# Performance work log

Measured on AMD Instinct MI355X. Metric: run time of the kernel, lower is better.

## Reference

```python
import jax, jax.numpy as jnp
import numpy as np
from jax import lax

K_NN = 16      # neighbors used by compute_knn_distance
ANCHOR_K = 64  # config['anchor_k']


def _knn_dist_vec(pts):
    """compute_knn_distance for one object: mean offset vector to K_NN nearest neighbors.
    pts: (N, 3) -> (N, 3)"""
    sq = jnp.sum(pts * pts, axis=-1)                      # (N,)
    d2 = sq[:, None] + sq[None, :] - 2.0 * (pts @ pts.T)  # (N, N) squared dists
    n = pts.shape[0]
    d2 = d2 + jnp.eye(n, dtype=pts.dtype) * 1e10          # exclude self
    _, idx = lax.top_k(-d2, K_NN)                          # (N, K_NN) nearest indices
    neigh = pts[idx]                                       # (N, K_NN, 3)
    return jnp.mean(neigh - pts[:, None, :], axis=1)       # (N, 3)


def _fps(pts, k):
    """Farthest point sampling for one object. pts: (N, 3) -> (k,) int32 indices."""
    d0 = jnp.sum((pts - pts[0]) ** 2, axis=-1)             # dist to seed point 0

    def step(min_d, _):
        idx = jnp.argmax(min_d)
        d = jnp.sum((pts - pts[idx]) ** 2, axis=-1)
        return jnp.minimum(min_d, d), idx

    _, idxs = lax.scan(step, d0, None, length=k - 1)
    return jnp.concatenate([jnp.zeros((1,), dtype=idxs.dtype), idxs])


def setup_inputs() -> dict:
    key = jax.random.key(0)
    k1, k2, k3, k4 = jax.random.split(key, 4)
    B, N_obj, N_v = 4, 8, 2048
    positions = jax.random.normal(k1, (B, N_obj, N_v, 3), dtype=jnp.float32)
    velocities = jax.random.normal(k2, (B, N_obj, N_v, 3), dtype=jnp.float32)
    physics_params = jax.random.uniform(k3, (B, N_obj, 3), dtype=jnp.float32)
    # reference pose at t=0: nearby but distinct so rel_pos is nontrivial
    ref_positions = positions + 0.05 * jax.random.normal(k4, (B, N_obj, N_v, 3), dtype=jnp.float32)
    return {"positions": positions, "velocities": velocities,
            "physics_params": physics_params, "ref_positions": ref_positions}


def reference(positions, velocities, physics_params, ref_positions):
    B, N_obj, N_v, _ = positions.shape
    flat = positions.reshape(B * N_obj, N_v, 3)

    # pairwise KNN distance feature per point
    dist_vec = jax.vmap(_knn_dist_vec)(flat).reshape(B, N_obj, N_v, 3)

    # iterative FPS anchor sampling (vectorized over all B*N_obj objects)
    anchors = jax.vmap(lambda p: _fps(p, ANCHOR_K))(flat).reshape(B, N_obj, ANCHOR_K)

    rel_pos = positions - ref_positions

    # multi-field gather at anchor indices (torch.gather on dim=2)
    gather = lambda f: jnp.take_along_axis(f, anchors[..., None], axis=2)
    anchor_dist = gather(dist_vec)       # (B, N_obj, K, 3)
    anchor_vel = gather(velocities)      # (B, N_obj, K, 3)
    anchor_rel = gather(rel_pos)         # (B, N_obj, K, 3)

    phys = jnp.broadcast_to(physics_params[:, :, None, :], (B, N_obj, ANCHOR_K, 3))
    query = jnp.concatenate([anchor_dist, anchor_vel, anchor_rel, phys], axis=-1)  # (B, N_obj, K, 12)
    return query
```

## Files before the change

kernel.cpp:

```cpp
#include <hip/hip_runtime.h>
#include <stdint.h>

#define NPTS 2048
#define KNN  16
#define AK   64
#define TPB  256
#define FPT  (NPTS / TPB)
#define KPL  (NPTS / 64)

typedef unsigned long long u64;
typedef unsigned int u32;
#define UMAX 0xFFFFFFFFFFFFFFFFull

__device__ __forceinline__ float sq3(float x, float y, float z) {
    return __fadd_rn(__fadd_rn(__fmul_rn(x, x), __fmul_rn(y, y)), __fmul_rn(z, z));
}

template <int CTRL>
__device__ __forceinline__ u64 dpp64(u64 k) {
    const int lo = __builtin_amdgcn_update_dpp((int)(u32)k, (int)(u32)k,
                                               CTRL, 0xF, 0xF, false);
    const int hi = __builtin_amdgcn_update_dpp((int)(u32)(k >> 32),
                                               (int)(u32)(k >> 32),
                                               CTRL, 0xF, 0xF, false);
    return ((u64)(u32)hi << 32) | (u32)lo;
}

__device__ __forceinline__ u64 wave_max64(u64 k) {
    u64 o;
    o = dpp64<0xB1>(k);  if (o > k) k = o;
    o = dpp64<0x4E>(k);  if (o > k) k = o;
    o = dpp64<0x141>(k); if (o > k) k = o;
    o = dpp64<0x140>(k); if (o > k) k = o;
    o = (u64)__shfl_xor((long long)k, 16, 64); if (o > k) k = o;
    o = (u64)__shfl_xor((long long)k, 32, 64); if (o > k) k = o;
    return k;
}

__device__ __forceinline__ u64 wave_min64(u64 k) {
    u64 o;
    o = dpp64<0xB1>(k);  if (o < k) k = o;
    o = dpp64<0x4E>(k);  if (o < k) k = o;
    o = dpp64<0x141>(k); if (o < k) k = o;
    o = dpp64<0x140>(k); if (o < k) k = o;
    o = (u64)__shfl_xor((long long)k, 16, 64); if (o < k) k = o;
    o = (u64)__shfl_xor((long long)k, 32, 64); if (o < k) k = o;
    return k;
}

__global__ __launch_bounds__(TPB) void fps_kernel(const float* __restrict__ pos,
                                                  int* __restrict__ anchors) {
    const int obj = blockIdx.x;
    const int t = threadIdx.x;
    const int wid = t >> 6, lane = t & 63;

    __shared__ float sX[NPTS], sY[NPTS], sZ[NPTS];
    __shared__ u64 skey[8];
    __shared__ float4 scrd[8];

    const float* pts = pos + (size_t)obj * NPTS * 3;
    #pragma unroll
    for (int i = 0; i < FPT; i++) {
        const int j = t + i * TPB;
        sX[j] = pts[j * 3 + 0];
        sY[j] = pts[j * 3 + 1];
        sZ[j] = pts[j * 3 + 2];
    }
    __syncthreads();

    float px[FPT], py[FPT], pz[FPT], mind[FPT];
    u64 key;
    {
        const float ax0 = sX[0], ay0 = sY[0], az0 = sZ[0];
        float bv = -1.0f; u32 bj = 0;
        #pragma unroll
        for (int i = 0; i < FPT; i++) {
            const int j = t + i * TPB;
            px[i] = sX[j]; py[i] = sY[j]; pz[i] = sZ[j];
            const float d2 = sq3(__fsub_rn(px[i], ax0), __fsub_rn(py[i], ay0),
                                 __fsub_rn(pz[i], az0));
            mind[i] = d2;
            if (d2 > bv) { bv = d2; bj = (u32)j; }
        }
        key = ((u64)__float_as_uint(bv) << 32) | (u32)(~bj);
    }
    if (t == 0) anchors[obj * AK + 0] = 0;

    for (int s = 1; s < AK; s++) {
        const u64 wk = wave_max64(key);
        const int side = (s & 1) * 4;
        if (lane == 0) {
            const int widx = (int)(~(u32)wk);
            skey[side + wid] = wk;
            scrd[side + wid] = make_float4(sX[widx], sY[widx], sZ[widx], 0.f);
        }
        __syncthreads();
        u64 ka = skey[side + 0];
        float4 ca = scrd[side + 0];
        { const u64 k1 = skey[side + 1]; const float4 q = scrd[side + 1];
          if (k1 > ka) { ka = k1; ca = q; } }
        { const u64 k2 = skey[side + 2]; const float4 q = scrd[side + 2];
          if (k2 > ka) { ka = k2; ca = q; } }
        { const u64 k3 = skey[side + 3]; const float4 q = scrd[side + 3];
          if (k3 > ka) { ka = k3; ca = q; } }
        if (t == 0) anchors[obj * AK + s] = (int)(~(u32)ka);
        if (s == AK - 1) break;

        float bv = -1.0f; u32 bj = 0;
        #pragma unroll
        for (int i = 0; i < FPT; i++) {
            const float d2 = sq3(__fsub_rn(px[i], ca.x), __fsub_rn(py[i], ca.y),
                                 __fsub_rn(pz[i], ca.z));
            const float nm = fminf(mind[i], d2);
            mind[i] = nm;
            if (nm > bv) { bv = nm; bj = (u32)(t + i * TPB); }
        }
        key = ((u64)__float_as_uint(bv) << 32) | (u32)(~bj);
    }
}

__global__ __launch_bounds__(TPB) void knn_gather_kernel(
    const float* __restrict__ pos, const float* __restrict__ vel,
    const float* __restrict__ phys, const float* __restrict__ refp,
    const int* __restrict__ anchors, float* __restrict__ out) {
    const int t = threadIdx.x;
    const int wid = t >> 6, lane = t & 63;
    const int g = blockIdx.x * 4 + wid;
    const int obj = g >> 6;

    __shared__ float sX[NPTS], sY[NPTS], sZ[NPTS];
    const float* pts = pos + (size_t)obj * NPTS * 3;
    #pragma unroll
    for (int i = 0; i < FPT; i++) {
        const int j = t + i * TPB;
        sX[j] = pts[j * 3 + 0];
        sY[j] = pts[j * 3 + 1];
        sZ[j] = pts[j * 3 + 2];
    }
    const int a = anchors[g];
    __syncthreads();

    const float ax = sX[a], ay = sY[a], az = sZ[a];
    const float sqa = sq3(ax, ay, az);

    u64 k[KPL];
    #pragma unroll
    for (int i = 0; i < KPL; i++) {
        const int j = lane + i * 64;
        const float x = sX[j], y = sY[j], z = sZ[j];
        const float sqj = sq3(x, y, z);
        const float dot = __fadd_rn(
            __fadd_rn(__fmul_rn(ax, x), __fmul_rn(ay, y)), __fmul_rn(az, z));
        const float d2 = __fsub_rn(__fadd_rn(sqa, sqj), __fmul_rn(2.0f, dot));
        u32 bb = __float_as_uint(d2);
        bb ^= (bb & 0x80000000u) ? 0xFFFFFFFFu : 0x80000000u;
        k[i] = (j == a) ? UMAX : (((u64)bb << 32) | (u32)j);
    }

    u64 c0 = UMAX, c1 = UMAX, c2 = UMAX, c3 = UMAX;
    #pragma unroll
    for (int i = 0; i < KPL; i++) c0 = (k[i] < c0) ? k[i] : c0;
    #pragma unroll
    for (int i = 0; i < KPL; i++) {
        const u64 v = (k[i] > c0) ? k[i] : UMAX; c1 = (v < c1) ? v : c1;
    }
    #pragma unroll
    for (int i = 0; i < KPL; i++) {
        const u64 v = (k[i] > c1) ? k[i] : UMAX; c2 = (v < c2) ? v : c2;
    }
    #pragma unroll
    for (int i = 0; i < KPL; i++) {
        const u64 v = (k[i] > c2) ? k[i] : UMAX; c3 = (v < c3) ? v : c3;
    }

    float accx = 0.f, accy = 0.f, accz = 0.f;
    u64 thr = 0;
    for (int r = 0; r < KNN; r++) {
        if (c0 == UMAX) {
            #pragma unroll
            for (int i = 0; i < KPL; i++) {
                const u64 v = (k[i] > thr) ? k[i] : UMAX; c0 = (v < c0) ? v : c0;
            }
            #pragma unroll
            for (int i = 0; i < KPL; i++) {
                const u64 v = (k[i] > c0) ? k[i] : UMAX; c1 = (v < c1) ? v : c1;
            }
            #pragma unroll
            for (int i = 0; i < KPL; i++) {
                const u64 v = (k[i] > c1) ? k[i] : UMAX; c2 = (v < c2) ? v : c2;
            }
            #pragma unroll
            for (int i = 0; i < KPL; i++) {
                const u64 v = (k[i] > c2) ? k[i] : UMAX; c3 = (v < c3) ? v : c3;
            }
        }
        const u64 w = wave_min64(c0);
        const int winj = (int)(u32)w;
        const float wx = sX[winj], wy = sY[winj], wz = sZ[winj];
        accx = __fadd_rn(accx, __fsub_rn(wx, ax));
        accy = __fadd_rn(accy, __fsub_rn(wy, ay));
        accz = __fadd_rn(accz, __fsub_rn(wz, az));
        if (c0 == w) {
            thr = c0; c0 = c1; c1 = c2; c2 = c3; c3 = UMAX;
        }
    }

    if (lane == 0) {
        float* o = out + (size_t)g * 12;
        o[0] = __fmul_rn(accx, 0.0625f);
        o[1] = __fmul_rn(accy, 0.0625f);
        o[2] = __fmul_rn(accz, 0.0625f);
        const size_t base = (size_t)obj * NPTS * 3 + (size_t)a * 3;
        o[3] = vel[base + 0];
        o[4] = vel[base + 1];
        o[5] = vel[base + 2];
        o[6] = __fsub_rn(pos[base + 0], refp[base + 0]);
        o[7] = __fsub_rn(pos[base + 1], refp[base + 1]);
        o[8] = __fsub_rn(pos[base + 2], refp[base + 2]);
        const float* ph = phys + (size_t)obj * 3;
        o[9]  = ph[0];
        o[10] = ph[1];
        o[11] = ph[2];
    }
}

extern "C" void kernel_launch(void* const* d_in, const int* in_sizes, int n_in,
                              void* d_out, int out_size, void* d_ws, size_t ws_size,
                              hipStream_t stream) {
    const float* pos  = (const float*)d_in[0];
    const float* vel  = (const float*)d_in[1];
    const float* phys = (const float*)d_in[2];
    const float* refp = (const float*)d_in[3];
    float* out = (float*)d_out;

    const int n_obj = in_sizes[2] / 3;
    int* anchors = (int*)d_ws;

    fps_kernel<<<n_obj, TPB, 0, stream>>>(pos, anchors);
    knn_gather_kernel<<<n_obj * AK / 4, TPB, 0, stream>>>(pos, vel, phys, refp,
                                                          anchors, out);
}
```

Measured before the change: 109.8 us.

## Run FPS in a single wavefront and use permlane swaps for wave reductions

FPS now runs with one 64-lane wavefront per object, with each lane holding 32 points in registers. The per-step cross-wave shared-memory exchange and __syncthreads disappear, and the chosen centre's coordinates come from an AoS float4 LDS table. The wave reductions use permlane16/32 swap builtins when available instead of shfl_xor. The KNN kernel stores float4 points with a precomputed squared norm and software-pipelines the winner coordinate fetch. The trade-off is that FPS has 4x fewer threads per object, so the serial 63-step chain does 4x more ALU work per lane.

```diff
diff --git a/kernel.cpp b/kernel.cpp
--- a/kernel.cpp
+++ b/kernel.cpp
@@ -7,6 +7,7 @@
 #define TPB  256
 #define FPT  (NPTS / TPB)
 #define KPL  (NPTS / 64)
+#define FW   (NPTS / 64)
 
 typedef unsigned long long u64;
 typedef unsigned int u32;
@@ -26,96 +27,106 @@
     return ((u64)(u32)hi << 32) | (u32)lo;
 }
 
+__device__ __forceinline__ void swap16_pair(u64 k, u64& a, u64& b) {
+#if __has_builtin(__builtin_amdgcn_permlane16_swap)
+    const u32 lo = (u32)k, hi = (u32)(k >> 32);
+    const auto rl = __builtin_amdgcn_permlane16_swap(lo, lo, false, false);
+    const auto rh = __builtin_amdgcn_permlane16_swap(hi, hi, false, false);
+    a = ((u64)(u32)rh[0] << 32) | (u32)rl[0];
+    b = ((u64)(u32)rh[1] << 32) | (u32)rl[1];
+#else
+    a = (u64)__shfl_xor((long long)k, 16, 64);
+    b = a;
+#endif
+}
+
+__device__ __forceinline__ void swap32_pair(u64 k, u64& a, u64& b) {
+#if __has_builtin(__builtin_amdgcn_permlane32_swap)
+    const u32 lo = (u32)k, hi = (u32)(k >> 32);
+    const auto rl = __builtin_amdgcn_permlane32_swap(lo, lo, false, false);
+    const auto rh = __builtin_amdgcn_permlane32_swap(hi, hi, false, false);
+    a = ((u64)(u32)rh[0] << 32) | (u32)rl[0];
+    b = ((u64)(u32)rh[1] << 32) | (u32)rl[1];
+#else
+    a = (u64)__shfl_xor((long long)k, 32, 64);
+    b = a;
+#endif
+}
+
 __device__ __forceinline__ u64 wave_max64(u64 k) {
-    u64 o;
+    u64 o, a, b;
     o = dpp64<0xB1>(k);  if (o > k) k = o;
     o = dpp64<0x4E>(k);  if (o > k) k = o;
     o = dpp64<0x141>(k); if (o > k) k = o;
     o = dpp64<0x140>(k); if (o > k) k = o;
-    o = (u64)__shfl_xor((long long)k, 16, 64); if (o > k) k = o;
-    o = (u64)__shfl_xor((long long)k, 32, 64); if (o > k) k = o;
+    swap16_pair(k, a, b); if (a > k) k = a; if (b > k) k = b;
+    swap32_pair(k, a, b); if (a > k) k = a; if (b > k) k = b;
     return k;
 }
 
 __device__ __forceinline__ u64 wave_min64(u64 k) {
-    u64 o;
+    u64 o, a, b;
     o = dpp64<0xB1>(k);  if (o < k) k = o;
     o = dpp64<0x4E>(k);  if (o < k) k = o;
     o = dpp64<0x141>(k); if (o < k) k = o;
     o = dpp64<0x140>(k); if (o < k) k = o;
-    o = (u64)__shfl_xor((long long)k, 16, 64); if (o < k) k = o;
-    o = (u64)__shfl_xor((long long)k, 32, 64); if (o < k) k = o;
+    swap16_pair(k, a, b); if (a < k) k = a; if (b < k) k = b;
+    swap32_pair(k, a, b); if (a < k) k = a; if (b < k) k = b;
     return k;
 }
 
-__global__ __launch_bounds__(TPB) void fps_kernel(const float* __restrict__ pos,
-                                                  int* __restrict__ anchors) {
+__global__ __launch_bounds__(64) void fps_kernel(const float* __restrict__ pos,
+                                                 int* __restrict__ anchors) {
     const int obj = blockIdx.x;
-    const int t = threadIdx.x;
-    const int wid = t >> 6, lane = t & 63;
-
-    __shared__ float sX[NPTS], sY[NPTS], sZ[NPTS];
-    __shared__ u64 skey[8];
-    __shared__ float4 scrd[8];
+    const int lane = threadIdx.x & 63;
+
+    __shared__ float4 sP[NPTS];
 
     const float* pts = pos + (size_t)obj * NPTS * 3;
-    #pragma unroll
-    for (int i = 0; i < FPT; i++) {
-        const int j = t + i * TPB;
-        sX[j] = pts[j * 3 + 0];
-        sY[j] = pts[j * 3 + 1];
-        sZ[j] = pts[j * 3 + 2];
-    }
-    __syncthreads();
-
-    float px[FPT], py[FPT], pz[FPT], mind[FPT];
-    u64 key;
-    {
-        const float ax0 = sX[0], ay0 = sY[0], az0 = sZ[0];
-        float bv = -1.0f; u32 bj = 0;
-        #pragma unroll
-        for (int i = 0; i < FPT; i++) {
-            const int j = t + i * TPB;
-            px[i] = sX[j]; py[i] = sY[j]; pz[i] = sZ[j];
-            const float d2 = sq3(__fsub_rn(px[i], ax0), __fsub_rn(py[i], ay0),
-                                 __fsub_rn(pz[i], az0));
-            mind[i] = d2;
-            if (d2 > bv) { bv = d2; bj = (u32)j; }
-        }
-        key = ((u64)__float_as_uint(bv) << 32) | (u32)(~bj);
-    }
-    if (t == 0) anchors[obj * AK + 0] = 0;
-
+    float px[FW], py[FW], pz[FW], mind[FW];
+    #pragma unroll
+    for (int i = 0; i < FW; i++) {
+        const int j = lane + i * 64;
+        const float x = pts[j * 3 + 0];
+        const float y = pts[j * 3 + 1];
+        const float z = pts[j * 3 + 2];
+        px[i] = x; py[i] = y; pz[i] = z;
+        sP[j] = make_float4(x, y, z, 0.f);
+    }
+    if (lane == 0) anchors[obj * AK + 0] = 0;
+
+    const float ax0 = __shfl(px[0], 0, 64);
+    const float ay0 = __shfl(py[0], 0, 64);
+    const float az0 = __shfl(pz[0], 0, 64);
+    float bv = -1.0f; u32 bj = 0;
+    #pragma unroll
+    for (int i = 0; i < FW; i++) {
+        const float d2 = sq3(__fsub_rn(px[i], ax0), __fsub_rn(py[i], ay0),
+                             __fsub_rn(pz[i], az0));
+        mind[i] = d2;
+        if (d2 > bv) { bv = d2; bj = (u32)(lane + i * 64); }
+    }
+    u64 key = ((u64)__float_as_uint(bv) << 32) | (u32)(~bj);
+
+    #pragma unroll 1
     for (int s = 1; s < AK; s++) {
         const u64 wk = wave_max64(key);
-        const int side = (s & 1) * 4;
-        if (lane == 0) {
-            const int widx = (int)(~(u32)wk);
-            skey[side + wid] = wk;
-            scrd[side + wid] = make_float4(sX[widx], sY[widx], sZ[widx], 0.f);
-        }
-        __syncthreads();
-        u64 ka = skey[side + 0];
-        float4 ca = scrd[side + 0];
-        { const u64 k1 = skey[side + 1]; const float4 q = scrd[side + 1];
-          if (k1 > ka) { ka = k1; ca = q; } }
-        { const u64 k2 = skey[side + 2]; const float4 q = scrd[side + 2];
-          if (k2 > ka) { ka = k2; ca = q; } }
-        { const u64 k3 = skey[side + 3]; const float4 q = scrd[side + 3];
-          if (k3 > ka) { ka = k3; ca = q; } }
-        if (t == 0) anchors[obj * AK + s] = (int)(~(u32)ka);
+        const int widx = (int)(~(u32)wk);
+        if (lane == 0) anchors[obj * AK + s] = widx;
         if (s == AK - 1) break;
 
-        float bv = -1.0f; u32 bj = 0;
+        const float4 c = sP[widx];
+
+        float nbv = -1.0f; u32 nbj = 0;
         #pragma unroll
-        for (int i = 0; i < FPT; i++) {
-            const float d2 = sq3(__fsub_rn(px[i], ca.x), __fsub_rn(py[i], ca.y),
-                                 __fsub_rn(pz[i], ca.z));
+        for (int i = 0; i < FW; i++) {
+            const float d2 = sq3(__fsub_rn(px[i], c.x), __fsub_rn(py[i], c.y),
+                                 __fsub_rn(pz[i], c.z));
             const float nm = fminf(mind[i], d2);
             mind[i] = nm;
-            if (nm > bv) { bv = nm; bj = (u32)(t + i * TPB); }
+            if (nm > nbv) { nbv = nm; nbj = (u32)(lane + i * 64); }
         }
-        key = ((u64)__float_as_uint(bv) << 32) | (u32)(~bj);
+        key = ((u64)__float_as_uint(nbv) << 32) | (u32)(~nbj);
     }
 }
 
@@ -128,30 +139,31 @@
     const int g = blockIdx.x * 4 + wid;
     const int obj = g >> 6;
 
-    __shared__ float sX[NPTS], sY[NPTS], sZ[NPTS];
+    __shared__ float4 sP[NPTS];
     const float* pts = pos + (size_t)obj * NPTS * 3;
     #pragma unroll
     for (int i = 0; i < FPT; i++) {
         const int j = t + i * TPB;
-        sX[j] = pts[j * 3 + 0];
-        sY[j] = pts[j * 3 + 1];
-        sZ[j] = pts[j * 3 + 2];
+        const float x = pts[j * 3 + 0];
+        const float y = pts[j * 3 + 1];
+        const float z = pts[j * 3 + 2];
+        sP[j] = make_float4(x, y, z, sq3(x, y, z));
     }
     const int a = anchors[g];
     __syncthreads();
 
-    const float ax = sX[a], ay = sY[a], az = sZ[a];
-    const float sqa = sq3(ax, ay, az);
+    const float4 ca = sP[a];
+    const float ax = ca.x, ay = ca.y, az = ca.z;
+    const float sqa = ca.w;
 
     u64 k[KPL];
     #pragma unroll
     for (int i = 0; i < KPL; i++) {
         const int j = lane + i * 64;
-        const float x = sX[j], y = sY[j], z = sZ[j];
-        const float sqj = sq3(x, y, z);
+        const float4 p = sP[j];
         const float dot = __fadd_rn(
-            __fadd_rn(__fmul_rn(ax, x), __fmul_rn(ay, y)), __fmul_rn(az, z));
-        const float d2 = __fsub_rn(__fadd_rn(sqa, sqj), __fmul_rn(2.0f, dot));
+            __fadd_rn(__fmul_rn(ax, p.x), __fmul_rn(ay, p.y)), __fmul_rn(az, p.z));
+        const float d2 = __fsub_rn(__fadd_rn(sqa, p.w), __fmul_rn(2.0f, dot));
         u32 bb = __float_as_uint(d2);
         bb ^= (bb & 0x80000000u) ? 0xFFFFFFFFu : 0x80000000u;
         k[i] = (j == a) ? UMAX : (((u64)bb << 32) | (u32)j);
@@ -175,7 +187,14 @@
 
     float accx = 0.f, accy = 0.f, accz = 0.f;
     u64 thr = 0;
-    for (int r = 0; r < KNN; r++) {
+    float4 cw;
+    {
+        const u64 w = wave_min64(c0);
+        cw = sP[(int)(u32)w];
+        if (c0 == w) { thr = c0; c0 = c1; c1 = c2; c2 = c3; c3 = UMAX; }
+    }
+    #pragma unroll 1
+    for (int r = 1; r < KNN; r++) {
         if (c0 == UMAX) {
             #pragma unroll
             for (int i = 0; i < KPL; i++) {
@@ -195,15 +214,18 @@
             }
         }
         const u64 w = wave_min64(c0);
-        const int winj = (int)(u32)w;
-        const float wx = sX[winj], wy = sY[winj], wz = sZ[winj];
-        accx = __fadd_rn(accx, __fsub_rn(wx, ax));
-        accy = __fadd_rn(accy, __fsub_rn(wy, ay));
-        accz = __fadd_rn(accz, __fsub_rn(wz, az));
+        const float4 cn = sP[(int)(u32)w];
+        accx = __fadd_rn(accx, __fsub_rn(cw.x, ax));
+        accy = __fadd_rn(accy, __fsub_rn(cw.y, ay));
+        accz = __fadd_rn(accz, __fsub_rn(cw.z, az));
+        cw = cn;
         if (c0 == w) {
             thr = c0; c0 = c1; c1 = c2; c2 = c3; c3 = UMAX;
         }
     }
+    accx = __fadd_rn(accx, __fsub_rn(cw.x, ax));
+    accy = __fadd_rn(accy, __fsub_rn(cw.y, ay));
+    accz = __fadd_rn(accz, __fsub_rn(cw.z, az));
 
     if (lane == 0) {
         float* o = out + (size_t)g * 12;
@@ -236,7 +258,7 @@
     const int n_obj = in_sizes[2] / 3;
     int* anchors = (int*)d_ws;
 
-    fps_kernel<<<n_obj, TPB, 0, stream>>>(pos, anchors);
+    fps_kernel<<<n_obj, 64, 0, stream>>>(pos, anchors);
     knn_gather_kernel<<<n_obj * AK / 4, TPB, 0, stream>>>(pos, vel, phys, refp,
                                                           anchors, out);
 }
```

After: 126.1 us. 14.9% more time.
